# Performance work log

Measured on AMD Instinct MI355X. Metric: run time of the kernel, lower is better.

The kernel has to match this reference:

```python
import jax, jax.numpy as jnp
import numpy as np

EM_STEPS = 2
C, N, H, F = 32, 200000, 4, 64


def setup_inputs() -> dict:
    key = jax.random.key(0)
    kq, kk, kv = jax.random.split(key, 3)
    Q = jax.random.normal(kq, (C, H, F), dtype=jnp.float32)
    K = jax.random.normal(kk, (N, H, F), dtype=jnp.float32)
    V = jax.random.normal(kv, (N, H, F), dtype=jnp.float32)
    return {"Q": Q, "K": K, "V": V}


def reference(Q, K, V):
    # EM-style recurrent cross-attention:
    #   scores[c,n,h] = sum_f centroid[c,h,f] * K[n,h,f] / sqrt(F)
    #   weights = softmax over clusters (axis 0)
    #   centroid[c,h,f] = sum_n weights[c,n,h] * V[n,h,f]
    scale = 1.0 / np.sqrt(np.float32(Q.shape[-1]))
    centroid = Q
    for _ in range(EM_STEPS):
        scores = jnp.einsum('chf,nhf->cnh', centroid, K) * scale  # (C,N,H)
        weights = jax.nn.softmax(scores, axis=0)                  # over clusters
        centroid = jnp.einsum('cnh,nhf->chf', weights, V)         # (C,H,F)
    return centroid
```

## Files before the change

### kernel.cpp

```cpp
#include <hip/hip_runtime.h>


#define CC 32
#define HH 4
#define FF 64
#define NB 64
#define WAVES 8
#define BLOCK 512
#define GX 128

typedef float f32x2 __attribute__((ext_vector_type(2)));

__device__ __forceinline__ void pkfma(f32x2& d, f32x2 a, f32x2 b) {
    asm("v_pk_fma_f32 %0, %1, %2, %0" : "+v"(d) : "v"(a), "v"(b));
}

__global__ __launch_bounds__(BLOCK, 4) void em_step_kernel(
    const float* __restrict__ cent_in,
    const float* __restrict__ Kp,
    const float* __restrict__ Vp,
    float* __restrict__ cent_out,
    int N)
{
    const int h    = blockIdx.y;
    const int tid  = threadIdx.x;
    const int wid  = tid >> 6;
    const int lane = tid & 63;

    __shared__ float centT[FF][CC];
    __shared__ float wlds[WAVES][NB][36];

    for (int i = tid; i < CC * FF; i += BLOCK) {
        int c = i & (CC - 1), f = i >> 5;
        centT[f][c] = cent_in[(c * HH + h) * FF + f] * 0.125f;
    }
    __syncthreads();

    f32x2 acc2[16];
    #pragma unroll
    for (int p = 0; p < 16; ++p) acc2[p] = f32x2{0.f, 0.f};

    const int ngroups = (N + NB - 1) / NB;

    for (int g = blockIdx.x * WAVES + wid; g < ngroups; g += GX * WAVES) {
        const int n0 = g * NB;

        const int  n     = n0 + lane;
        const bool valid = (n < N);
        const int  ncl   = valid ? n : (N - 1);
        const float4* Kr = (const float4*)(Kp + ((size_t)ncl * HH + h) * FF);

        f32x2 s2[16];
        #pragma unroll
        for (int p = 0; p < 16; ++p) s2[p] = f32x2{0.f, 0.f};

        #pragma unroll 4
        for (int f4 = 0; f4 < FF / 4; ++f4) {
            float4 k4 = Kr[f4];
            float kv[4] = {k4.x, k4.y, k4.z, k4.w};
            #pragma unroll
            for (int ff = 0; ff < 4; ++ff) {
                f32x2 kk = {kv[ff], kv[ff]};
                const float4* crow = (const float4*)&centT[f4 * 4 + ff][0];
                #pragma unroll
                for (int c8 = 0; c8 < 8; ++c8) {
                    float4 ce = crow[c8];
                    pkfma(s2[c8 * 2 + 0], kk, f32x2{ce.x, ce.y});
                    pkfma(s2[c8 * 2 + 1], kk, f32x2{ce.z, ce.w});
                }
            }
        }

        float m = -3.0e38f;
        #pragma unroll
        for (int p = 0; p < 16; ++p) m = fmaxf(m, fmaxf(s2[p].x, s2[p].y));
        float sum = 0.f;
        #pragma unroll
        for (int p = 0; p < 16; ++p) {
            s2[p].x = __expf(s2[p].x - m); sum += s2[p].x;
            s2[p].y = __expf(s2[p].y - m); sum += s2[p].y;
        }
        float r = 1.0f / sum;
        if (!valid) r = 0.f;

        float4* wr = (float4*)&wlds[wid][lane][0];
        #pragma unroll
        for (int c4 = 0; c4 < 8; ++c4) {
            float4 w4;
            w4.x = s2[2 * c4].x     * r;
            w4.y = s2[2 * c4].y     * r;
            w4.z = s2[2 * c4 + 1].x * r;
            w4.w = s2[2 * c4 + 1].y * r;
            wr[c4] = w4;
        }

        const float* Vb = Vp + (size_t)h * FF + lane;

        auto loadv = [&](float (&buf)[16], int jbase) {
            #pragma unroll
            for (int jj = 0; jj < 16; ++jj) {
                int nj  = n0 + jbase + jj;
                int njc = nj < N ? nj : (N - 1);
                buf[jj] = Vb[(size_t)njc * (HH * FF)];
            }
        };
        auto pv = [&](const float (&buf)[16], int jbase) {
            #pragma unroll
            for (int jj = 0; jj < 16; ++jj) {
                int j = jbase + jj;
                f32x2 vv = {buf[jj], buf[jj]};
                const float4* wrow = (const float4*)&wlds[wid][j][0];
                #pragma unroll
                for (int c4 = 0; c4 < 8; ++c4) {
                    float4 w4 = wrow[c4];
                    pkfma(acc2[2 * c4 + 0], vv, f32x2{w4.x, w4.y});
                    pkfma(acc2[2 * c4 + 1], vv, f32x2{w4.z, w4.w});
                }
            }
        };

        float va[16], vb[16];
        loadv(va, 0);
        loadv(vb, 16);
        pv(va, 0);
        loadv(va, 32);
        pv(vb, 16);
        loadv(vb, 48);
        pv(va, 32);
        pv(vb, 48);
    }

    __syncthreads();
    float* red = &wlds[0][0][0];
    #pragma unroll
    for (int p = 0; p < 16; ++p) {
        red[(wid * CC + 2 * p + 0) * FF + lane] = acc2[p].x;
        red[(wid * CC + 2 * p + 1) * FF + lane] = acc2[p].y;
    }
    __syncthreads();
    #pragma unroll
    for (int k = 0; k < (CC * FF) / BLOCK; ++k) {
        int o = k * BLOCK + tid;
        int c = o >> 6, f = o & 63;
        float val = 0.f;
        #pragma unroll
        for (int w = 0; w < WAVES; ++w) val += red[(w * CC + c) * FF + f];
        atomicAdd(&cent_out[(c * HH + h) * FF + f], val);
    }
}

extern "C" void kernel_launch(void* const* d_in, const int* in_sizes, int n_in,
                              void* d_out, int out_size, void* d_ws, size_t ws_size,
                              hipStream_t stream)
{
    const float* Q = (const float*)d_in[0];
    const float* K = (const float*)d_in[1];
    const float* V = (const float*)d_in[2];
    float*       out   = (float*)d_out;
    float*       cent1 = (float*)d_ws;

    const int N = in_sizes[1] / (HH * FF);

    hipMemsetAsync(cent1, 0, CC * HH * FF * sizeof(float), stream);
    hipMemsetAsync(out,   0, CC * HH * FF * sizeof(float), stream);

    dim3 grid(GX, HH), block(BLOCK);
    em_step_kernel<<<grid, block, 0, stream>>>(Q,     K, V, cent1, N);
    em_step_kernel<<<grid, block, 0, stream>>>(cent1, K, V, out,   N);
}
```

Before: 727.7 us.

## Software-pipeline K loads across groups and deepen V load double-buffering

Splits the K row load into four quarter loads that are issued ahead of the QK dot-product work on the previous quarter, and prefetches the first quarter of the next group during the PV phase. V loads are restructured into 8-row double buffers with a deeper interleaved schedule. Bounds checks and clamping are removed by assuming N is a multiple of 64, which drops tail handling; inputs where N is not a multiple of 64 would then give wrong results. The goal is to hide global memory latency behind FMA work, at the cost of more live registers.

Result: slower. 1.508 ms (+107.2%).

```diff
diff --git a/kernel.cpp b/kernel.cpp
--- a/kernel.cpp
+++ b/kernel.cpp
@@ -8,6 +8,7 @@
 #define WAVES 8
 #define BLOCK 512
 #define GX 128
+#define HF (HH * FF)
 
 typedef float f32x2 __attribute__((ext_vector_type(2)));
 
@@ -40,28 +41,26 @@
     #pragma unroll
     for (int p = 0; p < 16; ++p) acc2[p] = f32x2{0.f, 0.f};
 
-    const int ngroups = (N + NB - 1) / NB;
+    const int ngroups = N / NB;
+    const int gstep   = GX * WAVES;
+    const int g0      = blockIdx.x * WAVES + wid;
 
-    for (int g = blockIdx.x * WAVES + wid; g < ngroups; g += GX * WAVES) {
-        const int n0 = g * NB;
+    auto issueKq = [&](float4 (&kb)[4], int g, int quar) {
+        int gg = g < ngroups ? g : (ngroups - 1);
+        const float4* Kr =
+            (const float4*)(Kp + (gg * NB + lane) * HF + h * FF) + quar * 4;
+        #pragma unroll
+        for (int q = 0; q < 4; ++q) kb[q] = Kr[q];
+    };
 
-        const int  n     = n0 + lane;
-        const bool valid = (n < N);
-        const int  ncl   = valid ? n : (N - 1);
-        const float4* Kr = (const float4*)(Kp + ((size_t)ncl * HH + h) * FF);
-
-        f32x2 s2[16];
+    auto qkq = [&](const float4 (&kb)[4], int quar, f32x2 (&s2)[16]) {
         #pragma unroll
-        for (int p = 0; p < 16; ++p) s2[p] = f32x2{0.f, 0.f};
-
-        #pragma unroll 4
-        for (int f4 = 0; f4 < FF / 4; ++f4) {
-            float4 k4 = Kr[f4];
-            float kv[4] = {k4.x, k4.y, k4.z, k4.w};
+        for (int q = 0; q < 4; ++q) {
+            float kv[4] = {kb[q].x, kb[q].y, kb[q].z, kb[q].w};
             #pragma unroll
             for (int ff = 0; ff < 4; ++ff) {
                 f32x2 kk = {kv[ff], kv[ff]};
-                const float4* crow = (const float4*)&centT[f4 * 4 + ff][0];
+                const float4* crow = (const float4*)&centT[quar * 16 + q * 4 + ff][0];
                 #pragma unroll
                 for (int c8 = 0; c8 < 8; ++c8) {
                     float4 ce = crow[c8];
@@ -70,6 +69,25 @@
                 }
             }
         }
+    };
+
+    float4 kp0[4];
+    issueKq(kp0, g0, 0);
+
+    for (int g = g0; g < ngroups; g += gstep) {
+        float4 kq1[4], kq2[4], kq3[4];
+        issueKq(kq1, g, 1);
+
+        f32x2 s2[16];
+        #pragma unroll
+        for (int p = 0; p < 16; ++p) s2[p] = f32x2{0.f, 0.f};
+
+        qkq(kp0, 0, s2);
+        issueKq(kq2, g, 2);
+        qkq(kq1, 1, s2);
+        issueKq(kq3, g, 3);
+        qkq(kq2, 2, s2);
+        qkq(kq3, 3, s2);
 
         float m = -3.0e38f;
         #pragma unroll
@@ -81,7 +99,6 @@
             s2[p].y = __expf(s2[p].y - m); sum += s2[p].y;
         }
         float r = 1.0f / sum;
-        if (!valid) r = 0.f;
 
         float4* wr = (float4*)&wlds[wid][lane][0];
         #pragma unroll
@@ -94,22 +111,21 @@
             wr[c4] = w4;
         }
 
-        const float* Vb = Vp + (size_t)h * FF + lane;
+        issueKq(kp0, g + gstep, 0);
 
-        auto loadv = [&](float (&buf)[16], int jbase) {
+        const float* Vb = Vp + g * NB * HF + h * FF + lane;
+
+        float va[8], vb[8];
+        auto loadv = [&](float (&buf)[8], int jb) {
+            const float* p = Vb + jb * HF;
             #pragma unroll
-            for (int jj = 0; jj < 16; ++jj) {
-                int nj  = n0 + jbase + jj;
-                int njc = nj < N ? nj : (N - 1);
-                buf[jj] = Vb[(size_t)njc * (HH * FF)];
-            }
+            for (int jj = 0; jj < 8; ++jj) buf[jj] = p[jj * HF];
         };
-        auto pv = [&](const float (&buf)[16], int jbase) {
+        auto pv = [&](const float (&buf)[8], int jb) {
             #pragma unroll
-            for (int jj = 0; jj < 16; ++jj) {
-                int j = jbase + jj;
+            for (int jj = 0; jj < 8; ++jj) {
                 f32x2 vv = {buf[jj], buf[jj]};
-                const float4* wrow = (const float4*)&wlds[wid][j][0];
+                const float4* wrow = (const float4*)&wlds[wid][jb + jj][0];
                 #pragma unroll
                 for (int c4 = 0; c4 < 8; ++c4) {
                     float4 w4 = wrow[c4];
@@ -119,15 +135,15 @@
             }
         };
 
-        float va[16], vb[16];
         loadv(va, 0);
-        loadv(vb, 16);
-        pv(va, 0);
-        loadv(va, 32);
-        pv(vb, 16);
-        loadv(vb, 48);
-        pv(va, 32);
-        pv(vb, 48);
+        loadv(vb, 8);  pv(va, 0);
+        loadv(va, 16); pv(vb, 8);
+        loadv(vb, 24); pv(va, 16);
+        loadv(va, 32); pv(vb, 24);
+        loadv(vb, 40); pv(va, 32);
+        loadv(va, 48); pv(vb, 40);
+        loadv(vb, 56); pv(va, 48);
+        pv(vb, 56);
     }
 
     __syncthreads();
```
